# Kernel tuning notes

Measured on AMD Instinct MI355X. Metric: run time of the kernel, lower is better.

## Reference

```python
import jax, jax.numpy as jnp
from jax import lax
import numpy as np

B, T, F, H = 32, 512, 1024, 1024


def setup_inputs() -> dict:
    key = jax.random.key(0)
    ks = jax.random.split(key, 7)
    s = 0.02
    return {
        "x": jax.random.normal(ks[0], (B, T, F), dtype=jnp.float32),
        "W0": jax.random.normal(ks[1], (F, 4 * H), dtype=jnp.float32) * s,
        "U0": jax.random.normal(ks[2], (H, 4 * H), dtype=jnp.float32) * s,
        "b0": jax.random.normal(ks[3], (4 * H,), dtype=jnp.float32) * s,
        "W1": jax.random.normal(ks[4], (H, 4 * H), dtype=jnp.float32) * s,
        "U1": jax.random.normal(ks[5], (H, 4 * H), dtype=jnp.float32) * s,
        "b1": jax.random.normal(ks[6], (4 * H,), dtype=jnp.float32) * s,
    }


def _lstm(x, W, U, b):
    # x: [B, T, F] -> sequence outputs [B, T, H], final h, final c
    b_, t_, _ = x.shape
    h_dim = U.shape[0]
    # Precompute input projections for all timesteps (batched GEMM).
    xz = jnp.einsum('btf,fg->btg', x, W) + b  # [B, T, 4H]

    def step(carry, xz_t):
        h, c = carry
        z = xz_t + h @ U  # [B, 4H]
        i, f, g, o = jnp.split(z, 4, axis=-1)  # Keras gate order: i, f, c(g), o
        i = jax.nn.sigmoid(i)
        f = jax.nn.sigmoid(f)
        g = jnp.tanh(g)
        o = jax.nn.sigmoid(o)
        c = f * c + i * g
        h = o * jnp.tanh(c)
        return (h, c), h

    h0 = jnp.zeros((b_, h_dim), dtype=x.dtype)
    c0 = jnp.zeros((b_, h_dim), dtype=x.dtype)
    (h, c), hs = lax.scan(step, (h0, c0), jnp.swapaxes(xz, 0, 1))
    return jnp.swapaxes(hs, 0, 1), h, c


def reference(x, W0, U0, b0, W1, U1, b1):
    # Layer 0: return_sequences=True
    seq0, _, _ = _lstm(x, W0, U0, b0)
    # Layer 1: return_state=True -> (last_output, h, c); last_output == h
    _, h1, c1 = _lstm(seq0, W1, U1, b1)
    return (h1, h1, c1)
```

## Files before the change

### kernel.cpp

```cpp
#include <hip/hip_runtime.h>
#include <cstdint>


typedef __attribute__((ext_vector_type(8))) short bf16x8;
typedef __attribute__((ext_vector_type(4))) short s16x4;
typedef __attribute__((ext_vector_type(4))) float f32x4;
typedef __attribute__((ext_vector_type(2))) unsigned int u32x2;

#define XZ0_OFF   0ull
#define XF_OFF    134217728ull
#define W0F_OFF   167772160ull
#define U0F_OFF   176160768ull
#define W1F_OFF   184549376ull
#define WS_TOTAL  201326592ull
#define RING_OFF  XF_OFF
#define H1B_OFF   (XF_OFF + 524288ull)
#define FLG_OFF   (XF_OFF + 655360ull)

__device__ __forceinline__ float bf2f(short s) {
  unsigned int u = ((unsigned int)(unsigned short)s) << 16;
  return __builtin_bit_cast(float, u);
}
__device__ __forceinline__ short f2bf(float f) {
  unsigned int u = __builtin_bit_cast(unsigned int, f);
  u = (u + 0x7fffu + ((u >> 16) & 1u)) >> 16;
  return (short)u;
}
__device__ __forceinline__ void g2l16(const void* g, void* l) {
  __builtin_amdgcn_global_load_lds(
      (const __attribute__((address_space(1))) unsigned int*)g,
      (__attribute__((address_space(3))) unsigned int*)l, 16, 0, 0);
}
__device__ __forceinline__ float sigm(float x) { return 1.f / (1.f + __expf(-x)); }

__device__ __forceinline__ bf16x8 ld16_sc1(const short* p) {
  bf16x8 r;
  asm volatile("global_load_dwordx4 %0, %1, off sc1" : "=&v"(r) : "v"(p));
  return r;
}
__device__ __forceinline__ void st2_sc1(short* p, unsigned v) {
  asm volatile("global_store_short %0, %1, off sc1" :: "v"(p), "v"(v) : "memory");
}
__device__ __forceinline__ void st4_sc1(unsigned* p, unsigned v) {
  asm volatile("global_store_dword %0, %1, off sc1" :: "v"(p), "v"(v) : "memory");
}
#define VM_DRAIN asm volatile("s_waitcnt vmcnt(0)" ::: "memory")
#define SBAR __builtin_amdgcn_sched_barrier(0)

__global__ __launch_bounds__(256) void pack_x(const float* __restrict__ x,
                                              short* __restrict__ dst) {
  int gid = blockIdx.x * 256 + threadIdx.x;
  int lane = gid & 63;
  int unit = gid >> 6;
  int mtile = unit >> 5, kstep = unit & 31;
  int row = mtile * 16 + (lane & 15);
  int k0 = kstep * 32 + ((lane >> 4) << 3);
  const float* s = x + (size_t)row * 1024 + k0;
  bf16x8 v;
#pragma unroll
  for (int j = 0; j < 8; j++) v[j] = f2bf(s[j]);
  *(bf16x8*)(dst + (size_t)gid * 8) = v;
}

__global__ __launch_bounds__(256) void pack_w(const float* __restrict__ src0,
                                              const float* __restrict__ src1,
                                              int ksh, short* __restrict__ dst) {
  int gid = blockIdx.x * 256 + threadIdx.x;
  int lane = gid & 63;
  int unit = gid >> 6;
  int ntile = unit >> ksh;
  int kstep = unit & ((1 << ksh) - 1);
  int col = ntile * 16 + (lane & 15);
  int k0 = kstep * 32 + ((lane >> 4) << 3);
  const float* s = (k0 < 1024) ? src0 : src1;
  int kk = k0 & 1023;
  bf16x8 v;
#pragma unroll
  for (int j = 0; j < 8; j++) v[j] = f2bf(s[(size_t)(kk + j) * 4096 + col]);
  *(bf16x8*)(dst + (size_t)gid * 8) = v;
}

__global__ __launch_bounds__(256) void gemm_xw(const short* __restrict__ xf,
                                               const short* __restrict__ wf,
                                               short* __restrict__ outz) {
  extern __shared__ char smem[];

  int bid = blockIdx.x;
  int swz = (bid & 7) * 512 + (bid >> 3);
  int bn = swz >> 7;
  int bm = swz & 127;

  const int tid = threadIdx.x, wid = tid >> 6, lane = tid & 63;
  const int wm = wid >> 1, wn = wid & 1;
  f32x4 acc[4][4] = {};

  const short* xbase = xf + (size_t)(bm * 8) * 32 * 512;
  const short* wbase = wf + (size_t)(bn * 8) * 32 * 512;

  auto Abuf = [&](int buf) -> short* { return (short*)(smem + buf * 32768); };
  auto Bbuf = [&](int buf) -> short* { return (short*)(smem + 16384 + buf * 32768); };

  auto stage = [&](int buf, int kt) {
    short* A = Abuf(buf);
    short* B = Bbuf(buf);
#pragma unroll
    for (int i = 0; i < 4; i++) {
      int u = wid + 4 * i;
      int mt = u >> 1, ks = u & 1;
      int gk = kt * 2 + ks;
      g2l16(xbase + (size_t)(mt * 32 + gk) * 512 + lane * 8, A + u * 512);
      g2l16(wbase + (size_t)(mt * 32 + gk) * 512 + lane * 8, B + u * 512);
    }
  };

  stage(0, 0);
  __syncthreads();
  for (int kt = 0; kt < 16; kt++) {
    int buf = kt & 1;
    if (kt < 15) stage(buf ^ 1, kt + 1);
    const short* A = Abuf(buf) + (wm * 4) * 1024;
    const short* B = Bbuf(buf) + (wn * 4) * 1024;
#pragma unroll
    for (int ks = 0; ks < 2; ks++) {
      bf16x8 av[4], bv[4];
#pragma unroll
      for (int i = 0; i < 4; i++) av[i] = *(const bf16x8*)(A + (i * 2 + ks) * 512 + lane * 8);
#pragma unroll
      for (int j = 0; j < 4; j++) bv[j] = *(const bf16x8*)(B + (j * 2 + ks) * 512 + lane * 8);
#pragma unroll
      for (int i = 0; i < 4; i++)
#pragma unroll
        for (int j = 0; j < 4; j++)
          acc[i][j] = __builtin_amdgcn_mfma_f32_16x16x32_bf16(av[i], bv[j], acc[i][j], 0, 0, 0);
    }
    __syncthreads();
  }

  int rb = bm * 128 + wm * 64 + ((lane >> 4) << 2);
  int cb = bn * 128 + wn * 64 + (lane & 15);
#pragma unroll
  for (int i = 0; i < 4; i++)
#pragma unroll
    for (int j = 0; j < 4; j++)
#pragma unroll
      for (int r = 0; r < 4; r++) {
        size_t row = rb + i * 16 + r;
        int col = cb + j * 16;
        outz[row * 4096 + (size_t)(col & 1023) * 4 + (col >> 10)] = f2bf(acc[i][j][r]);
      }
}

__global__ __launch_bounds__(256, 1) void lstm_persist(
    const short* __restrict__ xz0, const short* __restrict__ u0f,
    const short* __restrict__ w1u1f, const float* __restrict__ b0,
    const float* __restrict__ b1, short* __restrict__ h0ring,
    short* __restrict__ h1buf, unsigned int* __restrict__ flags,
    float* __restrict__ out) {
  extern __shared__ char smem[];
  short* wlds = (short*)smem;
  float* red0 = (float*)(smem + 131072);
  float* red1 = (float*)(smem + 139264);

  const int wg = blockIdx.x;
  const int tid = threadIdx.x;
  const int wid = tid >> 6;
  const int lane = tid & 63;
  const bool l1 = (wg >= 128);
  const int u0 = (wg & 127) * 8;
  const int KS = l1 ? 64 : 32;
  const int ksh = l1 ? 6 : 5;
  const short* wf = l1 ? w1u1f : u0f;

  {
    int c = lane & 15;
    for (int u = wid; u < 2 * KS; u += 4) {
      int tau = u >> ksh;
      int s = u & (KS - 1);
      int gate = tau * 2 + (c >> 3);
      int gc = gate * 1024 + u0 + (c & 7);
      int lanep = (lane & 48) + (gc & 15);
      const short* src = wf + ((size_t)(((gc >> 4) << ksh) + s) * 64 + lanep) * 8;
      g2l16(src, wlds + (tau * KS + s) * 512);
    }
  }
  __syncthreads();

  const int bl = (tid & 127) >> 3;
  const int uu = tid & 7;
  const int lrow = bl >> 2, reg = bl & 3;
  float bias[4];
  {
    const float* bb = l1 ? b1 : b0;
#pragma unroll
    for (int g = 0; g < 4; g++) bias[g] = bb[g * 1024 + u0 + uu];
  }

  unsigned int* ownbase = flags + (l1 ? 256 : 0);
  unsigned int* othbase = flags + (l1 ? 0 : 256);

  auto pollq = [&](int q, unsigned own_t, unsigned oth_t) {
    if ((own_t | oth_t) == 0) return;
    const unsigned* po = ownbase + q * 128 + lane * 2;
    const unsigned* pe = othbase + q * 128 + lane * 2;
    for (int it = 0; it < (1 << 22); ++it) {
      u32x2 ov, ev;
      asm volatile(
          "global_load_dwordx2 %0, %2, off sc1\n\t"
          "global_load_dwordx2 %1, %3, off sc1\n\t"
          "s_waitcnt vmcnt(0)"
          : "=&v"(ov), "=&v"(ev)
          : "v"(po), "v"(pe)
          : "memory");
      if (__all(ov[0] >= own_t && ov[1] >= own_t &&
                ev[0] >= oth_t && ev[1] >= oth_t)) break;
      asm volatile("s_sleep 1");
    }
  };

  auto gates1 = [&](const float* rd, s16x4 xv, float& cst, short* hw,
                    bool dump, int g) {
    float z[4];
#pragma unroll
    for (int g4 = 0; g4 < 4; g4++) {
      int tau = g4 >> 1;
      int lp = lrow * 16 + (g4 & 1) * 8 + uu;
      float s = bias[g4] + bf2f(xv[g4]);
#pragma unroll
      for (int w4 = 0; w4 < 4; w4++)
        s += rd[((w4 * 2 + tau) * 64 + lp) * 4 + reg];
      z[g4] = s;
    }
    float gi = sigm(z[0]);
    float gf = sigm(z[1]);
    float gg = tanhf(z[2]);
    float go = sigm(z[3]);
    cst = gf * cst + gi * gg;
    float hv = go * tanhf(cst);
    st2_sc1(hw + (g * 16 + bl) * 1024 + u0 + uu,
            (unsigned)(unsigned short)f2bf(hv));
    if (dump) {
      int oi = (g * 16 + bl) * 1024 + u0 + uu;
      out[oi] = hv;
      out[32768 + oi] = hv;
      out[65536 + oi] = cst;
    }
  };

  if (!l1) {
    float c0 = 0.f, c1 = 0.f;
    auto mini = [&](int g, int t, float& cst) {
      const short* ap = h0ring + (size_t)((t - 1) & 7) * 32768 +
                        (g * 16 + (lane & 15)) * 1024 + (wid << 8) +
                        ((lane >> 4) << 3);
      bf16x8 a[8];
#pragma unroll
      for (int ks = 0; ks < 8; ks++) a[ks] = ld16_sc1(ap + ks * 32);
      s16x4 xv = {0, 0, 0, 0};
      if (tid < 128)
        xv = *(const s16x4*)(xz0 +
              ((size_t)((g * 16 + bl) * 512 + t) * 1024 + u0 + uu) * 4);
      SBAR; VM_DRAIN; SBAR;
      f32x4 acc[2] = {};
#pragma unroll
      for (int ks = 0; ks < 8; ks++) {
        bf16x8 bt0 = *(const bf16x8*)(wlds + (wid * 8 + ks) * 512 + lane * 8);
        bf16x8 bt1 = *(const bf16x8*)(wlds + (32 + wid * 8 + ks) * 512 + lane * 8);
        acc[0] = __builtin_amdgcn_mfma_f32_16x16x32_bf16(a[ks], bt0, acc[0], 0, 0, 0);
        acc[1] = __builtin_amdgcn_mfma_f32_16x16x32_bf16(a[ks], bt1, acc[1], 0, 0, 0);
      }
      float* rd = g ? red1 : red0;
#pragma unroll
      for (int tau = 0; tau < 2; tau++)
        *(f32x4*)(rd + ((wid * 2 + tau) * 64 + lane) * 4) = acc[tau];
      __syncthreads();
      if (tid < 128) {
        gates1(rd, xv, cst, h0ring + (size_t)(t & 7) * 32768, false, g);
      } else if (wid == 2 && g == 0) {
        pollq(1, (unsigned)t, (t >= 8) ? (unsigned)(t - 7) : 0u);
      } else if (wid == 3 && g == 1 && t < 511) {
        pollq(0, (unsigned)(t + 1), (t + 1 >= 8) ? (unsigned)(t - 6) : 0u);
      }
      VM_DRAIN;
      __syncthreads();
      if (tid == 0) st4_sc1(ownbase + g * 128 + (wg & 127), (unsigned)(t + 1));
    };
    for (int t = 0; t < 512; ++t) { mini(0, t, c0); mini(1, t, c1); }
  } else {
    float c0 = 0.f, c1 = 0.f;
    if (wid == 3) pollq(0, 0u, 1u);
    __syncthreads();
    auto mini = [&](int g, int t, float& cst) {
      const short* Ab = (wid < 2) ? (h0ring + (size_t)(t & 7) * 32768)
                                  : (h1buf + (size_t)((t - 1) & 1) * 32768);
      const short* ap = Ab + (g * 16 + (lane & 15)) * 1024 + ((wid & 1) << 9) +
                        ((lane >> 4) << 3);
      bf16x8 a[2][8];
#pragma unroll
      for (int half = 0; half < 2; half++)
#pragma unroll
        for (int ks = 0; ks < 8; ks++)
          a[half][ks] = ld16_sc1(ap + half * 256 + ks * 32);
      SBAR; VM_DRAIN; SBAR;
      f32x4 acc[2] = {};
#pragma unroll
      for (int half = 0; half < 2; half++) {
        const int rb = wid * 16 + half * 8;
#pragma unroll
        for (int ks = 0; ks < 8; ks++) {
          bf16x8 bt0 = *(const bf16x8*)(wlds + (rb + ks) * 512 + lane * 8);
          bf16x8 bt1 = *(const bf16x8*)(wlds + (64 + rb + ks) * 512 + lane * 8);
          acc[0] = __builtin_amdgcn_mfma_f32_16x16x32_bf16(a[half][ks], bt0, acc[0], 0, 0, 0);
          acc[1] = __builtin_amdgcn_mfma_f32_16x16x32_bf16(a[half][ks], bt1, acc[1], 0, 0, 0);
        }
      }
      float* rd = g ? red1 : red0;
#pragma unroll
      for (int tau = 0; tau < 2; tau++)
        *(f32x4*)(rd + ((wid * 2 + tau) * 64 + lane) * 4) = acc[tau];
      __syncthreads();
      if (tid < 128) {
        s16x4 zv = {0, 0, 0, 0};
        gates1(rd, zv, cst, h1buf + (size_t)(t & 1) * 32768, t == 511, g);
      } else if (wid == 2 && g == 0) {
        pollq(1, (unsigned)t, (unsigned)(t + 1));
      } else if (wid == 3 && g == 1 && t < 511) {
        pollq(0, (unsigned)(t + 1), (unsigned)(t + 2));
      }
      VM_DRAIN;
      __syncthreads();
      if (tid == 0) st4_sc1(ownbase + g * 128 + (wg & 127), (unsigned)(t + 1));
    };
    for (int t = 0; t < 512; ++t) { mini(0, t, c0); mini(1, t, c1); }
  }
}

extern "C" void kernel_launch(void* const* d_in, const int* in_sizes, int n_in,
                              void* d_out, int out_size, void* d_ws, size_t ws_size,
                              hipStream_t stream) {
  const float* x  = (const float*)d_in[0];
  const float* W0 = (const float*)d_in[1];
  const float* U0 = (const float*)d_in[2];
  const float* b0 = (const float*)d_in[3];
  const float* W1 = (const float*)d_in[4];
  const float* U1 = (const float*)d_in[5];
  const float* b1 = (const float*)d_in[6];
  char* ws = (char*)d_ws;
  if (ws_size < WS_TOTAL) return;

  short* xz0p = (short*)(ws + XZ0_OFF);
  short* xfp  = (short*)(ws + XF_OFF);
  short* w0fp = (short*)(ws + W0F_OFF);
  short* u0fp = (short*)(ws + U0F_OFF);
  short* w1fp = (short*)(ws + W1F_OFF);
  short* ringp = (short*)(ws + RING_OFF);
  short* h1p   = (short*)(ws + H1B_OFF);
  unsigned int* flagp = (unsigned int*)(ws + FLG_OFF);
  float* outp = (float*)d_out;

  (void)hipFuncSetAttribute((const void*)gemm_xw,
      hipFuncAttributeMaxDynamicSharedMemorySize, 65536);
  (void)hipFuncSetAttribute((const void*)lstm_persist,
      hipFuncAttributeMaxDynamicSharedMemorySize, 147456);

  hipLaunchKernelGGL(pack_x, dim3(8192), dim3(256), 0, stream, x, xfp);
  hipLaunchKernelGGL(pack_w, dim3(2048), dim3(256), 0, stream, W0, W0, 5, w0fp);
  hipLaunchKernelGGL(pack_w, dim3(2048), dim3(256), 0, stream, U0, U0, 5, u0fp);
  hipLaunchKernelGGL(pack_w, dim3(4096), dim3(256), 0, stream, W1, U1, 6, w1fp);
  hipLaunchKernelGGL(gemm_xw, dim3(4096), dim3(256), 65536, stream, xfp, w0fp, xz0p);

  (void)hipMemsetAsync(ws + RING_OFF, 0, 524288 + 131072 + 4096, stream);

  const short* xz0c = xz0p;
  const short* u0fc = u0fp;
  const short* w1fc = w1fp;
  void* kargs[9] = {(void*)&xz0c, (void*)&u0fc, (void*)&w1fc,
                    (void*)&b0,   (void*)&b1,
                    (void*)&ringp, (void*)&h1p, (void*)&flagp, (void*)&outp};
  (void)hipLaunchCooperativeKernel((const void*)lstm_persist, dim3(256), dim3(256),
                                   kargs, 147456u, stream);
}
```

Before: 3.919 ms.

## Prefetch next mini-step hidden-state loads before flag publish in LSTM recurrence

Restructures the per-timestep loop of both LSTM layers so that the A-operand (hidden state) loads for the next mini-step are issued right after the gate computation. Only the older stores are then drained with partial vmcnt waits, and raw s_barrier with lgkmcnt waits replaces full __syncthreads. Polling of neighbour progress flags moves to the start of each mini-step on wave 2, so the dependency wait sits right before use. The goal is to overlap global-load latency with the flag publish and barrier. The risk is subtle: the next loads are issued before the peers' flags have been checked, which can read stale ring data, and the hand-counted vmcnt values must match the number of outstanding ops exactly.

New measurement: 7.704 ms. +96.6%, slower.

```diff
diff --git a/kernel.cpp b/kernel.cpp
--- a/kernel.cpp
+++ b/kernel.cpp
@@ -38,6 +38,11 @@
   asm volatile("global_load_dwordx4 %0, %1, off sc1" : "=&v"(r) : "v"(p));
   return r;
 }
+__device__ __forceinline__ s16x4 ld8_plain(const short* p) {
+  s16x4 r;
+  asm volatile("global_load_dwordx2 %0, %1, off" : "=&v"(r) : "v"(p));
+  return r;
+}
 __device__ __forceinline__ void st2_sc1(short* p, unsigned v) {
   asm volatile("global_store_short %0, %1, off sc1" :: "v"(p), "v"(v) : "memory");
 }
@@ -45,7 +50,12 @@
   asm volatile("global_store_dword %0, %1, off sc1" :: "v"(p), "v"(v) : "memory");
 }
 #define VM_DRAIN asm volatile("s_waitcnt vmcnt(0)" ::: "memory")
+#define VM_W1    asm volatile("s_waitcnt vmcnt(1)" ::: "memory")
+#define VM_W9    asm volatile("s_waitcnt vmcnt(9)" ::: "memory")
+#define VM_W16   asm volatile("s_waitcnt vmcnt(16)" ::: "memory")
+#define LGKM0    asm volatile("s_waitcnt lgkmcnt(0)" ::: "memory")
 #define SBAR __builtin_amdgcn_sched_barrier(0)
+#define RBAR __builtin_amdgcn_s_barrier()
 
 __global__ __launch_bounds__(256) void pack_x(const float* __restrict__ x,
                                               short* __restrict__ dst) {
@@ -236,72 +246,91 @@
     float go = sigm(z[3]);
     cst = gf * cst + gi * gg;
     float hv = go * tanhf(cst);
-    st2_sc1(hw + (g * 16 + bl) * 1024 + u0 + uu,
-            (unsigned)(unsigned short)f2bf(hv));
     if (dump) {
       int oi = (g * 16 + bl) * 1024 + u0 + uu;
       out[oi] = hv;
       out[32768 + oi] = hv;
       out[65536 + oi] = cst;
     }
+    st2_sc1(hw + (g * 16 + bl) * 1024 + u0 + uu,
+            (unsigned)(unsigned short)f2bf(hv));
   };
 
   if (!l1) {
-    float c0 = 0.f, c1 = 0.f;
-    auto mini = [&](int g, int t, float& cst) {
+    bf16x8 A[8];
+    s16x4 xv = {0, 0, 0, 0};
+    auto issueA = [&](int g, int t) {
       const short* ap = h0ring + (size_t)((t - 1) & 7) * 32768 +
                         (g * 16 + (lane & 15)) * 1024 + (wid << 8) +
                         ((lane >> 4) << 3);
-      bf16x8 a[8];
-#pragma unroll
-      for (int ks = 0; ks < 8; ks++) a[ks] = ld16_sc1(ap + ks * 32);
-      s16x4 xv = {0, 0, 0, 0};
+#pragma unroll
+      for (int ks = 0; ks < 8; ks++) A[ks] = ld16_sc1(ap + ks * 32);
       if (tid < 128)
-        xv = *(const s16x4*)(xz0 +
-              ((size_t)((g * 16 + bl) * 512 + t) * 1024 + u0 + uu) * 4);
-      SBAR; VM_DRAIN; SBAR;
-      f32x4 acc[2] = {};
+        xv = ld8_plain(xz0 +
+             ((size_t)((g * 16 + bl) * 512 + t) * 1024 + u0 + uu) * 4);
+    };
+    auto body = [&](int g, int t, float& cst, int pq, unsigned po, unsigned pt,
+                    bool donext, int ng, int nt, bool first) {
+      if (wid == 2) pollq(pq, po, pt);
+      if (first) { VM_DRAIN; }
+      else if (wid == 0) { VM_W1; }
+      else { VM_DRAIN; }
+      SBAR;
+      f32x4 acc0 = {}, acc1 = {};
 #pragma unroll
       for (int ks = 0; ks < 8; ks++) {
         bf16x8 bt0 = *(const bf16x8*)(wlds + (wid * 8 + ks) * 512 + lane * 8);
         bf16x8 bt1 = *(const bf16x8*)(wlds + (32 + wid * 8 + ks) * 512 + lane * 8);
-        acc[0] = __builtin_amdgcn_mfma_f32_16x16x32_bf16(a[ks], bt0, acc[0], 0, 0, 0);
-        acc[1] = __builtin_amdgcn_mfma_f32_16x16x32_bf16(a[ks], bt1, acc[1], 0, 0, 0);
+        acc0 = __builtin_amdgcn_mfma_f32_16x16x32_bf16(A[ks], bt0, acc0, 0, 0, 0);
+        acc1 = __builtin_amdgcn_mfma_f32_16x16x32_bf16(A[ks], bt1, acc1, 0, 0, 0);
       }
       float* rd = g ? red1 : red0;
-#pragma unroll
-      for (int tau = 0; tau < 2; tau++)
-        *(f32x4*)(rd + ((wid * 2 + tau) * 64 + lane) * 4) = acc[tau];
-      __syncthreads();
+      *(f32x4*)(rd + ((wid * 2 + 0) * 64 + lane) * 4) = acc0;
+      *(f32x4*)(rd + ((wid * 2 + 1) * 64 + lane) * 4) = acc1;
+      LGKM0; RBAR; SBAR;
+      s16x4 xcur = xv;
       if (tid < 128) {
-        gates1(rd, xv, cst, h0ring + (size_t)(t & 7) * 32768, false, g);
-      } else if (wid == 2 && g == 0) {
-        pollq(1, (unsigned)t, (t >= 8) ? (unsigned)(t - 7) : 0u);
-      } else if (wid == 3 && g == 1 && t < 511) {
-        pollq(0, (unsigned)(t + 1), (t + 1 >= 8) ? (unsigned)(t - 6) : 0u);
+        gates1(rd, xcur, cst, h0ring + (size_t)(t & 7) * 32768, false, g);
+        if (donext) issueA(ng, nt);
+      } else {
+        if (donext) issueA(ng, nt);
       }
-      VM_DRAIN;
-      __syncthreads();
-      if (tid == 0) st4_sc1(ownbase + g * 128 + (wg & 127), (unsigned)(t + 1));
+      if (donext) { VM_W9; } else { VM_DRAIN; }
+      SBAR; RBAR;
+      if (tid == 0)
+        st4_sc1(ownbase + g * 128 + (wg & 127), (unsigned)(t + 1));
     };
-    for (int t = 0; t < 512; ++t) { mini(0, t, c0); mini(1, t, c1); }
+    issueA(0, 0);
+    float c0 = 0.f, c1 = 0.f;
+    for (int t = 0; t < 512; ++t) {
+      body(0, t, c0, 1, (unsigned)t, (t >= 8) ? (unsigned)(t - 7) : 0u,
+           true, 1, t, t == 0);
+      bool dn = (t < 511);
+      body(1, t, c1, 0, dn ? (unsigned)(t + 1) : 0u,
+           dn ? ((t + 1 >= 8) ? (unsigned)(t - 6) : 0u) : 0u,
+           dn, 0, t + 1, false);
+    }
   } else {
-    float c0 = 0.f, c1 = 0.f;
-    if (wid == 3) pollq(0, 0u, 1u);
-    __syncthreads();
-    auto mini = [&](int g, int t, float& cst) {
+    bf16x8 A1[2][8];
+    auto issueA1 = [&](int g, int t) {
       const short* Ab = (wid < 2) ? (h0ring + (size_t)(t & 7) * 32768)
                                   : (h1buf + (size_t)((t - 1) & 1) * 32768);
       const short* ap = Ab + (g * 16 + (lane & 15)) * 1024 + ((wid & 1) << 9) +
                         ((lane >> 4) << 3);
-      bf16x8 a[2][8];
 #pragma unroll
       for (int half = 0; half < 2; half++)
 #pragma unroll
         for (int ks = 0; ks < 8; ks++)
-          a[half][ks] = ld16_sc1(ap + half * 256 + ks * 32);
-      SBAR; VM_DRAIN; SBAR;
-      f32x4 acc[2] = {};
+          A1[half][ks] = ld16_sc1(ap + half * 256 + ks * 32);
+    };
+    auto body = [&](int g, int t, float& cst, int pq, unsigned po, unsigned pt,
+                    bool donext, int ng, int nt, bool first) {
+      if (wid == 2) pollq(pq, po, pt);
+      if (first) { VM_DRAIN; }
+      else if (wid == 0) { VM_W1; }
+      else { VM_DRAIN; }
+      SBAR;
+      f32x4 acc0 = {}, acc1 = {};
 #pragma unroll
       for (int half = 0; half < 2; half++) {
         const int rb = wid * 16 + half * 8;
@@ -309,28 +338,36 @@
         for (int ks = 0; ks < 8; ks++) {
           bf16x8 bt0 = *(const bf16x8*)(wlds + (rb + ks) * 512 + lane * 8);
           bf16x8 bt1 = *(const bf16x8*)(wlds + (64 + rb + ks) * 512 + lane * 8);
-          acc[0] = __builtin_amdgcn_mfma_f32_16x16x32_bf16(a[half][ks], bt0, acc[0], 0, 0, 0);
-          acc[1] = __builtin_amdgcn_mfma_f32_16x16x32_bf16(a[half][ks], bt1, acc[1], 0, 0, 0);
+          acc0 = __builtin_amdgcn_mfma_f32_16x16x32_bf16(A1[half][ks], bt0, acc0, 0, 0, 0);
+          acc1 = __builtin_amdgcn_mfma_f32_16x16x32_bf16(A1[half][ks], bt1, acc1, 0, 0, 0);
         }
       }
       float* rd = g ? red1 : red0;
-#pragma unroll
-      for (int tau = 0; tau < 2; tau++)
-        *(f32x4*)(rd + ((wid * 2 + tau) * 64 + lane) * 4) = acc[tau];
-      __syncthreads();
+      *(f32x4*)(rd + ((wid * 2 + 0) * 64 + lane) * 4) = acc0;
+      *(f32x4*)(rd + ((wid * 2 + 1) * 64 + lane) * 4) = acc1;
+      LGKM0; RBAR; SBAR;
       if (tid < 128) {
         s16x4 zv = {0, 0, 0, 0};
         gates1(rd, zv, cst, h1buf + (size_t)(t & 1) * 32768, t == 511, g);
-      } else if (wid == 2 && g == 0) {
-        pollq(1, (unsigned)t, (unsigned)(t + 1));
-      } else if (wid == 3 && g == 1 && t < 511) {
-        pollq(0, (unsigned)(t + 1), (unsigned)(t + 2));
+        if (donext) issueA1(ng, nt);
+      } else {
+        if (donext) issueA1(ng, nt);
       }
-      VM_DRAIN;
-      __syncthreads();
-      if (tid == 0) st4_sc1(ownbase + g * 128 + (wg & 127), (unsigned)(t + 1));
+      if (donext) { VM_W16; } else { VM_DRAIN; }
+      SBAR; RBAR;
+      if (tid == 0)
+        st4_sc1(ownbase + g * 128 + (wg & 127), (unsigned)(t + 1));
     };
-    for (int t = 0; t < 512; ++t) { mini(0, t, c0); mini(1, t, c1); }
+    if (wid == 2) pollq(0, 0u, 1u);
+    __syncthreads();
+    issueA1(0, 0);
+    float c0 = 0.f, c1 = 0.f;
+    for (int t = 0; t < 512; ++t) {
+      body(0, t, c0, 1, (unsigned)t, (unsigned)(t + 1), true, 1, t, t == 0);
+      bool dn = (t < 511);
+      body(1, t, c1, 0, dn ? (unsigned)(t + 1) : 0u,
+           dn ? (unsigned)(t + 2) : 0u, dn, 0, t + 1, false);
+    }
   }
 }
 
```

## Merge two batch half-steps into one full-batch step per timestep

Applied to the files above, without the earlier changes.

The persistent LSTM kernel used to process each timestep as two 16-row batch halves, each with its own flag publish and poll round. It now handles all 32 batch rows in a single pass per timestep, with four MFMA accumulators per wave and one flag set per layer. Layer 1 also waits on only the first half of its loads before starting MFMAs. This halves the number of cross-workgroup synchronisation rounds per step at the cost of more registers and less overlap between the two halves. Polling now happens after the flag store instead of overlapping with the gate computation.

Result: slower. 5.687 ms (+45.1%).

```diff
diff --git a/kernel.cpp b/kernel.cpp
--- a/kernel.cpp
+++ b/kernel.cpp
@@ -38,6 +38,11 @@
   asm volatile("global_load_dwordx4 %0, %1, off sc1" : "=&v"(r) : "v"(p));
   return r;
 }
+__device__ __forceinline__ s16x4 ld8_plain(const short* p) {
+  s16x4 r;
+  asm volatile("global_load_dwordx2 %0, %1, off" : "=&v"(r) : "v"(p));
+  return r;
+}
 __device__ __forceinline__ void st2_sc1(short* p, unsigned v) {
   asm volatile("global_store_short %0, %1, off sc1" :: "v"(p), "v"(v) : "memory");
 }
@@ -45,7 +50,16 @@
   asm volatile("global_store_dword %0, %1, off sc1" :: "v"(p), "v"(v) : "memory");
 }
 #define VM_DRAIN asm volatile("s_waitcnt vmcnt(0)" ::: "memory")
+#define VM_W16   asm volatile("s_waitcnt vmcnt(16)" ::: "memory")
 #define SBAR __builtin_amdgcn_sched_barrier(0)
+
+struct Frag8 { bf16x8 f0, f1, f2, f3, f4, f5, f6, f7; };
+#define LD8(F, B) do { \
+  (F).f0 = ld16_sc1((B));       (F).f1 = ld16_sc1((B) + 32);  \
+  (F).f2 = ld16_sc1((B) + 64);  (F).f3 = ld16_sc1((B) + 96);  \
+  (F).f4 = ld16_sc1((B) + 128); (F).f5 = ld16_sc1((B) + 160); \
+  (F).f6 = ld16_sc1((B) + 192); (F).f7 = ld16_sc1((B) + 224); \
+} while (0)
 
 __global__ __launch_bounds__(256) void pack_x(const float* __restrict__ x,
                                               short* __restrict__ dst) {
@@ -158,8 +172,7 @@
     float* __restrict__ out) {
   extern __shared__ char smem[];
   short* wlds = (short*)smem;
-  float* red0 = (float*)(smem + 131072);
-  float* red1 = (float*)(smem + 139264);
+  float* red = (float*)(smem + 131072);
 
   const int wg = blockIdx.x;
   const int tid = threadIdx.x;
@@ -185,23 +198,24 @@
   }
   __syncthreads();
 
-  const int bl = (tid & 127) >> 3;
-  const int uu = tid & 7;
-  const int lrow = bl >> 2, reg = bl & 3;
+  const int un = tid & 7;
+  const int r1 = (tid & 127) >> 3;
+  const int r2 = r1 + 16;
   float bias[4];
   {
     const float* bb = l1 ? b1 : b0;
 #pragma unroll
-    for (int g = 0; g < 4; g++) bias[g] = bb[g * 1024 + u0 + uu];
+    for (int g4 = 0; g4 < 4; g4++) bias[g4] = bb[g4 * 1024 + u0 + un];
   }
-
-  unsigned int* ownbase = flags + (l1 ? 256 : 0);
-  unsigned int* othbase = flags + (l1 ? 0 : 256);
-
-  auto pollq = [&](int q, unsigned own_t, unsigned oth_t) {
+  float cA = 0.f, cB = 0.f;
+
+  unsigned int* ownf = flags + (l1 ? 128 : 0);
+  unsigned int* othf = flags + (l1 ? 0 : 128);
+
+  auto pollq = [&](unsigned own_t, unsigned oth_t) {
     if ((own_t | oth_t) == 0) return;
-    const unsigned* po = ownbase + q * 128 + lane * 2;
-    const unsigned* pe = othbase + q * 128 + lane * 2;
+    const unsigned* po = ownf + lane * 2;
+    const unsigned* pe = othf + lane * 2;
     for (int it = 0; it < (1 << 22); ++it) {
       u32x2 ov, ev;
       asm volatile(
@@ -217,17 +231,18 @@
     }
   };
 
-  auto gates1 = [&](const float* rd, s16x4 xv, float& cst, short* hw,
-                    bool dump, int g) {
+  auto gaterow = [&](int r, s16x4 xv, float& cst, short* hw, bool dump) {
+    const int mt = r >> 4, bl = r & 15;
+    const int reg = bl & 3;
     float z[4];
 #pragma unroll
     for (int g4 = 0; g4 < 4; g4++) {
       int tau = g4 >> 1;
-      int lp = lrow * 16 + (g4 & 1) * 8 + uu;
+      int lp = (bl >> 2) * 16 + (g4 & 1) * 8 + un;
       float s = bias[g4] + bf2f(xv[g4]);
 #pragma unroll
       for (int w4 = 0; w4 < 4; w4++)
-        s += rd[((w4 * 2 + tau) * 64 + lp) * 4 + reg];
+        s += red[((w4 * 4 + mt * 2 + tau) * 64 + lp) * 4 + reg];
       z[g4] = s;
     }
     float gi = sigm(z[0]);
@@ -236,101 +251,123 @@
     float go = sigm(z[3]);
     cst = gf * cst + gi * gg;
     float hv = go * tanhf(cst);
-    st2_sc1(hw + (g * 16 + bl) * 1024 + u0 + uu,
-            (unsigned)(unsigned short)f2bf(hv));
     if (dump) {
-      int oi = (g * 16 + bl) * 1024 + u0 + uu;
+      int oi = r * 1024 + u0 + un;
       out[oi] = hv;
       out[32768 + oi] = hv;
       out[65536 + oi] = cst;
     }
+    st2_sc1(hw + r * 1024 + u0 + un, (unsigned)(unsigned short)f2bf(hv));
   };
 
   if (!l1) {
-    float c0 = 0.f, c1 = 0.f;
-    auto mini = [&](int g, int t, float& cst) {
+    for (int t = 0; t < 512; ++t) {
       const short* ap = h0ring + (size_t)((t - 1) & 7) * 32768 +
-                        (g * 16 + (lane & 15)) * 1024 + (wid << 8) +
-                        ((lane >> 4) << 3);
-      bf16x8 a[8];
-#pragma unroll
-      for (int ks = 0; ks < 8; ks++) a[ks] = ld16_sc1(ap + ks * 32);
-      s16x4 xv = {0, 0, 0, 0};
-      if (tid < 128)
-        xv = *(const s16x4*)(xz0 +
-              ((size_t)((g * 16 + bl) * 512 + t) * 1024 + u0 + uu) * 4);
+                        (lane & 15) * 1024 + (wid << 8) + ((lane >> 4) << 3);
+      Frag8 Fa, Fb;
+      LD8(Fa, ap);
+      LD8(Fb, ap + 16384);
+      s16x4 xvA = {0, 0, 0, 0}, xvB = {0, 0, 0, 0};
+      if (tid < 128) {
+        xvA = ld8_plain(xz0 + ((size_t)(r1 * 512 + t) * 1024 + u0 + un) * 4);
+        xvB = ld8_plain(xz0 + ((size_t)(r2 * 512 + t) * 1024 + u0 + un) * 4);
+      }
       SBAR; VM_DRAIN; SBAR;
-      f32x4 acc[2] = {};
+      f32x4 a00 = {}, a01 = {}, a10 = {}, a11 = {};
 #pragma unroll
       for (int ks = 0; ks < 8; ks++) {
         bf16x8 bt0 = *(const bf16x8*)(wlds + (wid * 8 + ks) * 512 + lane * 8);
         bf16x8 bt1 = *(const bf16x8*)(wlds + (32 + wid * 8 + ks) * 512 + lane * 8);
-        acc[0] = __builtin_amdgcn_mfma_f32_16x16x32_bf16(a[ks], bt0, acc[0], 0, 0, 0);
-        acc[1] = __builtin_amdgcn_mfma_f32_16x16x32_bf16(a[ks], bt1, acc[1], 0, 0, 0);
-      }
-      float* rd = g ? red1 : red0;
-#pragma unroll
-      for (int tau = 0; tau < 2; tau++)
-        *(f32x4*)(rd + ((wid * 2 + tau) * 64 + lane) * 4) = acc[tau];
+        bf16x8 fa = ks == 0 ? Fa.f0 : ks == 1 ? Fa.f1 : ks == 2 ? Fa.f2 :
+                    ks == 3 ? Fa.f3 : ks == 4 ? Fa.f4 : ks == 5 ? Fa.f5 :
+                    ks == 6 ? Fa.f6 : Fa.f7;
+        bf16x8 fb = ks == 0 ? Fb.f0 : ks == 1 ? Fb.f1 : ks == 2 ? Fb.f2 :
+                    ks == 3 ? Fb.f3 : ks == 4 ? Fb.f4 : ks == 5 ? Fb.f5 :
+                    ks == 6 ? Fb.f6 : Fb.f7;
+        a00 = __builtin_amdgcn_mfma_f32_16x16x32_bf16(fa, bt0, a00, 0, 0, 0);
+        a01 = __builtin_amdgcn_mfma_f32_16x16x32_bf16(fa, bt1, a01, 0, 0, 0);
+        a10 = __builtin_amdgcn_mfma_f32_16x16x32_bf16(fb, bt0, a10, 0, 0, 0);
+        a11 = __builtin_amdgcn_mfma_f32_16x16x32_bf16(fb, bt1, a11, 0, 0, 0);
+      }
+      *(f32x4*)(red + ((wid * 4 + 0) * 64 + lane) * 4) = a00;
+      *(f32x4*)(red + ((wid * 4 + 1) * 64 + lane) * 4) = a01;
+      *(f32x4*)(red + ((wid * 4 + 2) * 64 + lane) * 4) = a10;
+      *(f32x4*)(red + ((wid * 4 + 3) * 64 + lane) * 4) = a11;
       __syncthreads();
       if (tid < 128) {
-        gates1(rd, xv, cst, h0ring + (size_t)(t & 7) * 32768, false, g);
-      } else if (wid == 2 && g == 0) {
-        pollq(1, (unsigned)t, (t >= 8) ? (unsigned)(t - 7) : 0u);
-      } else if (wid == 3 && g == 1 && t < 511) {
-        pollq(0, (unsigned)(t + 1), (t + 1 >= 8) ? (unsigned)(t - 6) : 0u);
-      }
-      VM_DRAIN;
-      __syncthreads();
-      if (tid == 0) st4_sc1(ownbase + g * 128 + (wg & 127), (unsigned)(t + 1));
-    };
-    for (int t = 0; t < 512; ++t) { mini(0, t, c0); mini(1, t, c1); }
+        short* hw = h0ring + (size_t)(t & 7) * 32768;
+        gaterow(r1, xvA, cA, hw, false);
+        gaterow(r2, xvB, cB, hw, false);
+      }
+      __syncthreads();
+      if (tid == 0) st4_sc1(ownf + (wg & 127), (unsigned)(t + 1));
+      if (wid == 2 && t < 511)
+        pollq((unsigned)(t + 1), (t + 1 >= 8) ? (unsigned)(t - 6) : 0u);
+      __syncthreads();
+    }
   } else {
-    float c0 = 0.f, c1 = 0.f;
-    if (wid == 3) pollq(0, 0u, 1u);
+    if (wid == 2) pollq(0u, 1u);
     __syncthreads();
-    auto mini = [&](int g, int t, float& cst) {
+    for (int t = 0; t < 512; ++t) {
       const short* Ab = (wid < 2) ? (h0ring + (size_t)(t & 7) * 32768)
                                   : (h1buf + (size_t)((t - 1) & 1) * 32768);
-      const short* ap = Ab + (g * 16 + (lane & 15)) * 1024 + ((wid & 1) << 9) +
+      const short* ap = Ab + (lane & 15) * 1024 + ((wid & 1) << 9) +
                         ((lane >> 4) << 3);
-      bf16x8 a[2][8];
-#pragma unroll
-      for (int half = 0; half < 2; half++)
-#pragma unroll
-        for (int ks = 0; ks < 8; ks++)
-          a[half][ks] = ld16_sc1(ap + half * 256 + ks * 32);
+      Frag8 Fa, Fb, Fc, Fd;
+      LD8(Fa, ap);
+      LD8(Fb, ap + 16384);
+      LD8(Fc, ap + 256);
+      LD8(Fd, ap + 256 + 16384);
+      SBAR; VM_W16; SBAR;
+      f32x4 a00 = {}, a01 = {}, a10 = {}, a11 = {};
+#pragma unroll
+      for (int ks = 0; ks < 8; ks++) {
+        bf16x8 bt0 = *(const bf16x8*)(wlds + (wid * 16 + ks) * 512 + lane * 8);
+        bf16x8 bt1 = *(const bf16x8*)(wlds + (64 + wid * 16 + ks) * 512 + lane * 8);
+        bf16x8 fa = ks == 0 ? Fa.f0 : ks == 1 ? Fa.f1 : ks == 2 ? Fa.f2 :
+                    ks == 3 ? Fa.f3 : ks == 4 ? Fa.f4 : ks == 5 ? Fa.f5 :
+                    ks == 6 ? Fa.f6 : Fa.f7;
+        bf16x8 fb = ks == 0 ? Fb.f0 : ks == 1 ? Fb.f1 : ks == 2 ? Fb.f2 :
+                    ks == 3 ? Fb.f3 : ks == 4 ? Fb.f4 : ks == 5 ? Fb.f5 :
+                    ks == 6 ? Fb.f6 : Fb.f7;
+        a00 = __builtin_amdgcn_mfma_f32_16x16x32_bf16(fa, bt0, a00, 0, 0, 0);
+        a01 = __builtin_amdgcn_mfma_f32_16x16x32_bf16(fa, bt1, a01, 0, 0, 0);
+        a10 = __builtin_amdgcn_mfma_f32_16x16x32_bf16(fb, bt0, a10, 0, 0, 0);
+        a11 = __builtin_amdgcn_mfma_f32_16x16x32_bf16(fb, bt1, a11, 0, 0, 0);
+      }
       SBAR; VM_DRAIN; SBAR;
-      f32x4 acc[2] = {};
-#pragma unroll
-      for (int half = 0; half < 2; half++) {
-        const int rb = wid * 16 + half * 8;
-#pragma unroll
-        for (int ks = 0; ks < 8; ks++) {
-          bf16x8 bt0 = *(const bf16x8*)(wlds + (rb + ks) * 512 + lane * 8);
-          bf16x8 bt1 = *(const bf16x8*)(wlds + (64 + rb + ks) * 512 + lane * 8);
-          acc[0] = __builtin_amdgcn_mfma_f32_16x16x32_bf16(a[half][ks], bt0, acc[0], 0, 0, 0);
-          acc[1] = __builtin_amdgcn_mfma_f32_16x16x32_bf16(a[half][ks], bt1, acc[1], 0, 0, 0);
-        }
-      }
-      float* rd = g ? red1 : red0;
-#pragma unroll
-      for (int tau = 0; tau < 2; tau++)
-        *(f32x4*)(rd + ((wid * 2 + tau) * 64 + lane) * 4) = acc[tau];
+#pragma unroll
+      for (int ks = 0; ks < 8; ks++) {
+        bf16x8 bt0 = *(const bf16x8*)(wlds + (wid * 16 + 8 + ks) * 512 + lane * 8);
+        bf16x8 bt1 = *(const bf16x8*)(wlds + (64 + wid * 16 + 8 + ks) * 512 + lane * 8);
+        bf16x8 fc = ks == 0 ? Fc.f0 : ks == 1 ? Fc.f1 : ks == 2 ? Fc.f2 :
+                    ks == 3 ? Fc.f3 : ks == 4 ? Fc.f4 : ks == 5 ? Fc.f5 :
+                    ks == 6 ? Fc.f6 : Fc.f7;
+        bf16x8 fd = ks == 0 ? Fd.f0 : ks == 1 ? Fd.f1 : ks == 2 ? Fd.f2 :
+                    ks == 3 ? Fd.f3 : ks == 4 ? Fd.f4 : ks == 5 ? Fd.f5 :
+                    ks == 6 ? Fd.f6 : Fd.f7;
+        a00 = __builtin_amdgcn_mfma_f32_16x16x32_bf16(fc, bt0, a00, 0, 0, 0);
+        a01 = __builtin_amdgcn_mfma_f32_16x16x32_bf16(fc, bt1, a01, 0, 0, 0);
+        a10 = __builtin_amdgcn_mfma_f32_16x16x32_bf16(fd, bt0, a10, 0, 0, 0);
+        a11 = __builtin_amdgcn_mfma_f32_16x16x32_bf16(fd, bt1, a11, 0, 0, 0);
+      }
+      *(f32x4*)(red + ((wid * 4 + 0) * 64 + lane) * 4) = a00;
+      *(f32x4*)(red + ((wid * 4 + 1) * 64 + lane) * 4) = a01;
+      *(f32x4*)(red + ((wid * 4 + 2) * 64 + lane) * 4) = a10;
+      *(f32x4*)(red + ((wid * 4 + 3) * 64 + lane) * 4) = a11;
       __syncthreads();
       if (tid < 128) {
+        short* hw = h1buf + (size_t)(t & 1) * 32768;
         s16x4 zv = {0, 0, 0, 0};
-        gates1(rd, zv, cst, h1buf + (size_t)(t & 1) * 32768, t == 511, g);
-      } else if (wid == 2 && g == 0) {
-        pollq(1, (unsigned)t, (unsigned)(t + 1));
-      } else if (wid == 3 && g == 1 && t < 511) {
-        pollq(0, (unsigned)(t + 1), (unsigned)(t + 2));
-      }
-      VM_DRAIN;
-      __syncthreads();
-      if (tid == 0) st4_sc1(ownbase + g * 128 + (wg & 127), (unsigned)(t + 1));
-    };
-    for (int t = 0; t < 512; ++t) { mini(0, t, c0); mini(1, t, c1); }
+        gaterow(r1, zv, cA, hw, t == 511);
+        gaterow(r2, zv, cB, hw, t == 511);
+      }
+      __syncthreads();
+      if (tid == 0) st4_sc1(ownf + (wg & 127), (unsigned)(t + 1));
+      if (wid == 2 && t < 511)
+        pollq((unsigned)(t + 1), (unsigned)(t + 2));
+      __syncthreads();
+    }
   }
 }
 
```

## Replace block-level flag barriers with per-wave flags and 8-deep layer-1 ring

Applied to the files above, without the earlier changes.

Each wavefront now publishes its own completion flag and polls only the producer flags it needs before loading its slice of h. This removes the second __syncthreads per mini-step and the dedicated polling waves. Layer 1's h buffer grows from double-buffered to an 8-deep ring, so layer 0 can run further ahead. Gate computation is spread across all four waves (32 lanes each) instead of two. In exchange there are four times as many flag stores and more polling traffic, and the finer-grained memory ordering carries correctness risk.

After: 4.868 ms. +24.2%, slower.

```diff
diff --git a/kernel.cpp b/kernel.cpp
--- a/kernel.cpp
+++ b/kernel.cpp
@@ -6,6 +6,7 @@
 typedef __attribute__((ext_vector_type(4))) short s16x4;
 typedef __attribute__((ext_vector_type(4))) float f32x4;
 typedef __attribute__((ext_vector_type(2))) unsigned int u32x2;
+typedef __attribute__((ext_vector_type(4))) unsigned int u32x4;
 
 #define XZ0_OFF   0ull
 #define XF_OFF    134217728ull
@@ -13,9 +14,9 @@
 #define U0F_OFF   176160768ull
 #define W1F_OFF   184549376ull
 #define WS_TOTAL  201326592ull
-#define RING_OFF  XF_OFF
-#define H1B_OFF   (XF_OFF + 524288ull)
-#define FLG_OFF   (XF_OFF + 655360ull)
+#define H0R_OFF   XF_OFF
+#define H1R_OFF   (XF_OFF + 524288ull)
+#define FLG_OFF   (XF_OFF + 1048576ull)
 
 __device__ __forceinline__ float bf2f(short s) {
   unsigned int u = ((unsigned int)(unsigned short)s) << 16;
@@ -38,6 +39,11 @@
   asm volatile("global_load_dwordx4 %0, %1, off sc1" : "=&v"(r) : "v"(p));
   return r;
 }
+__device__ __forceinline__ s16x4 ld8_plain(const short* p) {
+  s16x4 r;
+  asm volatile("global_load_dwordx2 %0, %1, off" : "=&v"(r) : "v"(p));
+  return r;
+}
 __device__ __forceinline__ void st2_sc1(short* p, unsigned v) {
   asm volatile("global_store_short %0, %1, off sc1" :: "v"(p), "v"(v) : "memory");
 }
@@ -46,6 +52,17 @@
 }
 #define VM_DRAIN asm volatile("s_waitcnt vmcnt(0)" ::: "memory")
 #define SBAR __builtin_amdgcn_sched_barrier(0)
+
+struct Frag8 { bf16x8 f0, f1, f2, f3, f4, f5, f6, f7; };
+#define LD8(F, B) do { \
+  (F).f0 = ld16_sc1((B));       (F).f1 = ld16_sc1((B) + 32);  \
+  (F).f2 = ld16_sc1((B) + 64);  (F).f3 = ld16_sc1((B) + 96);  \
+  (F).f4 = ld16_sc1((B) + 128); (F).f5 = ld16_sc1((B) + 160); \
+  (F).f6 = ld16_sc1((B) + 192); (F).f7 = ld16_sc1((B) + 224); \
+} while (0)
+#define FSEL(F, ks) (ks == 0 ? (F).f0 : ks == 1 ? (F).f1 : ks == 2 ? (F).f2 : \
+                     ks == 3 ? (F).f3 : ks == 4 ? (F).f4 : ks == 5 ? (F).f5 : \
+                     ks == 6 ? (F).f6 : (F).f7)
 
 __global__ __launch_bounds__(256) void pack_x(const float* __restrict__ x,
                                               short* __restrict__ dst) {
@@ -154,7 +171,7 @@
     const short* __restrict__ xz0, const short* __restrict__ u0f,
     const short* __restrict__ w1u1f, const float* __restrict__ b0,
     const float* __restrict__ b1, short* __restrict__ h0ring,
-    short* __restrict__ h1buf, unsigned int* __restrict__ flags,
+    short* __restrict__ h1ring, unsigned int* __restrict__ flags,
     float* __restrict__ out) {
   extern __shared__ char smem[];
   short* wlds = (short*)smem;
@@ -163,7 +180,7 @@
 
   const int wg = blockIdx.x;
   const int tid = threadIdx.x;
-  const int wid = tid >> 6;
+  const int w = tid >> 6;
   const int lane = tid & 63;
   const bool l1 = (wg >= 128);
   const int u0 = (wg & 127) * 8;
@@ -173,7 +190,7 @@
 
   {
     int c = lane & 15;
-    for (int u = wid; u < 2 * KS; u += 4) {
+    for (int u = w; u < 2 * KS; u += 4) {
       int tau = u >> ksh;
       int s = u & (KS - 1);
       int gate = tau * 2 + (c >> 3);
@@ -185,49 +202,65 @@
   }
   __syncthreads();
 
-  const int bl = (tid & 127) >> 3;
-  const int uu = tid & 7;
-  const int lrow = bl >> 2, reg = bl & 3;
+  const int un = lane & 7;
   float bias[4];
   {
     const float* bb = l1 ? b1 : b0;
 #pragma unroll
-    for (int g = 0; g < 4; g++) bias[g] = bb[g * 1024 + u0 + uu];
+    for (int g4 = 0; g4 < 4; g4++) bias[g4] = bb[g4 * 1024 + u0 + un];
   }
 
-  unsigned int* ownbase = flags + (l1 ? 256 : 0);
-  unsigned int* othbase = flags + (l1 ? 0 : 256);
-
-  auto pollq = [&](int q, unsigned own_t, unsigned oth_t) {
-    if ((own_t | oth_t) == 0) return;
-    const unsigned* po = ownbase + q * 128 + lane * 2;
-    const unsigned* pe = othbase + q * 128 + lane * 2;
+  auto poll0 = [&](int g, int t) {
+    if (t == 0) return;
+    const unsigned tgt = (unsigned)t;
+    const unsigned lagt = (t >= 8) ? (unsigned)(t - 7) : 0u;
+    const unsigned* pp = flags + (unsigned)(g * 128 + w * 32) * 4 + lane * 2;
+    const unsigned* pl = flags + (unsigned)((2 + g) * 128 + w * 32 + (lane >> 1)) * 4 + (lane & 1);
     for (int it = 0; it < (1 << 22); ++it) {
-      u32x2 ov, ev;
+      u32x2 ov; unsigned lv;
       asm volatile(
           "global_load_dwordx2 %0, %2, off sc1\n\t"
-          "global_load_dwordx2 %1, %3, off sc1\n\t"
+          "global_load_dword %1, %3, off sc1\n\t"
           "s_waitcnt vmcnt(0)"
-          : "=&v"(ov), "=&v"(ev)
-          : "v"(po), "v"(pe)
-          : "memory");
-      if (__all(ov[0] >= own_t && ov[1] >= own_t &&
-                ev[0] >= oth_t && ev[1] >= oth_t)) break;
+          : "=&v"(ov), "=&v"(lv) : "v"(pp), "v"(pl) : "memory");
+      if (__all(ov[0] >= tgt && ov[1] >= tgt && lv >= lagt)) break;
       asm volatile("s_sleep 1");
     }
   };
-
-  auto gates1 = [&](const float* rd, s16x4 xv, float& cst, short* hw,
-                    bool dump, int g) {
+  auto poll1 = [&](int g, int t) {
+    unsigned tgt;
+    const unsigned* pp;
+    if (w < 2) {
+      tgt = (unsigned)(t + 1);
+      pp = flags + (unsigned)(g * 128 + w * 64) * 4 + lane * 4;
+    } else {
+      if (t == 0) return;
+      tgt = (unsigned)t;
+      pp = flags + (unsigned)((2 + g) * 128 + (w - 2) * 64) * 4 + lane * 4;
+    }
+    for (int it = 0; it < (1 << 22); ++it) {
+      u32x4 v;
+      asm volatile(
+          "global_load_dwordx4 %0, %1, off sc1\n\t"
+          "s_waitcnt vmcnt(0)"
+          : "=&v"(v) : "v"(pp) : "memory");
+      if (__all(v[0] >= tgt && v[1] >= tgt && v[2] >= tgt && v[3] >= tgt)) break;
+      asm volatile("s_sleep 1");
+    }
+  };
+
+  auto gates = [&](const float* rd, s16x4 xv, float& cst, short* hw,
+                   bool dump, int g) {
+    const int bl = w * 4 + (lane >> 3);
     float z[4];
 #pragma unroll
     for (int g4 = 0; g4 < 4; g4++) {
       int tau = g4 >> 1;
-      int lp = lrow * 16 + (g4 & 1) * 8 + uu;
+      int lp = (bl >> 2) * 16 + (g4 & 1) * 8 + un;
       float s = bias[g4] + bf2f(xv[g4]);
 #pragma unroll
       for (int w4 = 0; w4 < 4; w4++)
-        s += rd[((w4 * 2 + tau) * 64 + lp) * 4 + reg];
+        s += rd[((w4 * 2 + tau) * 64 + lp) * 4 + (bl & 3)];
       z[g4] = s;
     }
     float gi = sigm(z[0]);
@@ -236,99 +269,96 @@
     float go = sigm(z[3]);
     cst = gf * cst + gi * gg;
     float hv = go * tanhf(cst);
-    st2_sc1(hw + (g * 16 + bl) * 1024 + u0 + uu,
-            (unsigned)(unsigned short)f2bf(hv));
     if (dump) {
-      int oi = (g * 16 + bl) * 1024 + u0 + uu;
+      int oi = (g * 16 + bl) * 1024 + u0 + un;
       out[oi] = hv;
       out[32768 + oi] = hv;
       out[65536 + oi] = cst;
     }
+    st2_sc1(hw + (g * 16 + bl) * 1024 + u0 + un,
+            (unsigned)(unsigned short)f2bf(hv));
+  };
+
+  auto release = [&](int g, int t) {
+    if (lane == 0)
+      st4_sc1(flags + (unsigned)(((l1 ? 2 : 0) + g) * 128 + (wg & 127)) * 4 + w,
+              (unsigned)(t + 1));
   };
 
   if (!l1) {
     float c0 = 0.f, c1 = 0.f;
     auto mini = [&](int g, int t, float& cst) {
+      poll0(g, t);
       const short* ap = h0ring + (size_t)((t - 1) & 7) * 32768 +
-                        (g * 16 + (lane & 15)) * 1024 + (wid << 8) +
+                        (g * 16 + (lane & 15)) * 1024 + (w << 8) +
                         ((lane >> 4) << 3);
-      bf16x8 a[8];
-#pragma unroll
-      for (int ks = 0; ks < 8; ks++) a[ks] = ld16_sc1(ap + ks * 32);
+      Frag8 Fa;
+      LD8(Fa, ap);
       s16x4 xv = {0, 0, 0, 0};
-      if (tid < 128)
-        xv = *(const s16x4*)(xz0 +
-              ((size_t)((g * 16 + bl) * 512 + t) * 1024 + u0 + uu) * 4);
+      if (lane < 32) {
+        int bl = w * 4 + (lane >> 3);
+        xv = ld8_plain(xz0 +
+             (((size_t)((g * 16 + bl) * 512 + t)) * 1024 + u0 + un) * 4);
+      }
       SBAR; VM_DRAIN; SBAR;
-      f32x4 acc[2] = {};
+      f32x4 a0 = {}, a1 = {};
 #pragma unroll
       for (int ks = 0; ks < 8; ks++) {
-        bf16x8 bt0 = *(const bf16x8*)(wlds + (wid * 8 + ks) * 512 + lane * 8);
-        bf16x8 bt1 = *(const bf16x8*)(wlds + (32 + wid * 8 + ks) * 512 + lane * 8);
-        acc[0] = __builtin_amdgcn_mfma_f32_16x16x32_bf16(a[ks], bt0, acc[0], 0, 0, 0);
-        acc[1] = __builtin_amdgcn_mfma_f32_16x16x32_bf16(a[ks], bt1, acc[1], 0, 0, 0);
+        bf16x8 bt0 = *(const bf16x8*)(wlds + (w * 8 + ks) * 512 + lane * 8);
+        bf16x8 bt1 = *(const bf16x8*)(wlds + (32 + w * 8 + ks) * 512 + lane * 8);
+        bf16x8 fa = FSEL(Fa, ks);
+        a0 = __builtin_amdgcn_mfma_f32_16x16x32_bf16(fa, bt0, a0, 0, 0, 0);
+        a1 = __builtin_amdgcn_mfma_f32_16x16x32_bf16(fa, bt1, a1, 0, 0, 0);
       }
       float* rd = g ? red1 : red0;
-#pragma unroll
-      for (int tau = 0; tau < 2; tau++)
-        *(f32x4*)(rd + ((wid * 2 + tau) * 64 + lane) * 4) = acc[tau];
+      *(f32x4*)(rd + ((w * 2 + 0) * 64 + lane) * 4) = a0;
+      *(f32x4*)(rd + ((w * 2 + 1) * 64 + lane) * 4) = a1;
       __syncthreads();
-      if (tid < 128) {
-        gates1(rd, xv, cst, h0ring + (size_t)(t & 7) * 32768, false, g);
-      } else if (wid == 2 && g == 0) {
-        pollq(1, (unsigned)t, (t >= 8) ? (unsigned)(t - 7) : 0u);
-      } else if (wid == 3 && g == 1 && t < 511) {
-        pollq(0, (unsigned)(t + 1), (t + 1 >= 8) ? (unsigned)(t - 6) : 0u);
-      }
+      if (lane < 32)
+        gates(rd, xv, cst, h0ring + (size_t)(t & 7) * 32768, false, g);
       VM_DRAIN;
-      __syncthreads();
-      if (tid == 0) st4_sc1(ownbase + g * 128 + (wg & 127), (unsigned)(t + 1));
+      release(g, t);
     };
     for (int t = 0; t < 512; ++t) { mini(0, t, c0); mini(1, t, c1); }
   } else {
     float c0 = 0.f, c1 = 0.f;
-    if (wid == 3) pollq(0, 0u, 1u);
-    __syncthreads();
     auto mini = [&](int g, int t, float& cst) {
-      const short* Ab = (wid < 2) ? (h0ring + (size_t)(t & 7) * 32768)
-                                  : (h1buf + (size_t)((t - 1) & 1) * 32768);
-      const short* ap = Ab + (g * 16 + (lane & 15)) * 1024 + ((wid & 1) << 9) +
+      poll1(g, t);
+      const short* Ab = (w < 2) ? (h0ring + (size_t)(t & 7) * 32768)
+                                : (h1ring + (size_t)((t - 1) & 7) * 32768);
+      const short* ap = Ab + (g * 16 + (lane & 15)) * 1024 + ((w & 1) << 9) +
                         ((lane >> 4) << 3);
-      bf16x8 a[2][8];
-#pragma unroll
-      for (int half = 0; half < 2; half++)
-#pragma unroll
-        for (int ks = 0; ks < 8; ks++)
-          a[half][ks] = ld16_sc1(ap + half * 256 + ks * 32);
+      Frag8 Fa, Fc;
+      LD8(Fa, ap);
+      LD8(Fc, ap + 256);
       SBAR; VM_DRAIN; SBAR;
-      f32x4 acc[2] = {};
-#pragma unroll
-      for (int half = 0; half < 2; half++) {
-        const int rb = wid * 16 + half * 8;
-#pragma unroll
-        for (int ks = 0; ks < 8; ks++) {
-          bf16x8 bt0 = *(const bf16x8*)(wlds + (rb + ks) * 512 + lane * 8);
-          bf16x8 bt1 = *(const bf16x8*)(wlds + (64 + rb + ks) * 512 + lane * 8);
-          acc[0] = __builtin_amdgcn_mfma_f32_16x16x32_bf16(a[half][ks], bt0, acc[0], 0, 0, 0);
-          acc[1] = __builtin_amdgcn_mfma_f32_16x16x32_bf16(a[half][ks], bt1, acc[1], 0, 0, 0);
-        }
+      f32x4 a0 = {}, a1 = {};
+#pragma unroll
+      for (int ks = 0; ks < 8; ks++) {
+        bf16x8 bt0 = *(const bf16x8*)(wlds + (w * 16 + ks) * 512 + lane * 8);
+        bf16x8 bt1 = *(const bf16x8*)(wlds + (64 + w * 16 + ks) * 512 + lane * 8);
+        bf16x8 fa = FSEL(Fa, ks);
+        a0 = __builtin_amdgcn_mfma_f32_16x16x32_bf16(fa, bt0, a0, 0, 0, 0);
+        a1 = __builtin_amdgcn_mfma_f32_16x16x32_bf16(fa, bt1, a1, 0, 0, 0);
+      }
+#pragma unroll
+      for (int ks = 0; ks < 8; ks++) {
+        bf16x8 bt0 = *(const bf16x8*)(wlds + (w * 16 + 8 + ks) * 512 + lane * 8);
+        bf16x8 bt1 = *(const bf16x8*)(wlds + (64 + w * 16 + 8 + ks) * 512 + lane * 8);
+        bf16x8 fc = FSEL(Fc, ks);
+        a0 = __builtin_amdgcn_mfma_f32_16x16x32_bf16(fc, bt0, a0, 0, 0, 0);
+        a1 = __builtin_amdgcn_mfma_f32_16x16x32_bf16(fc, bt1, a1, 0, 0, 0);
       }
       float* rd = g ? red1 : red0;
-#pragma unroll
-      for (int tau = 0; tau < 2; tau++)
-        *(f32x4*)(rd + ((wid * 2 + tau) * 64 + lane) * 4) = acc[tau];
+      *(f32x4*)(rd + ((w * 2 + 0) * 64 + lane) * 4) = a0;
+      *(f32x4*)(rd + ((w * 2 + 1) * 64 + lane) * 4) = a1;
       __syncthreads();
-      if (tid < 128) {
+      if (lane < 32) {
         s16x4 zv = {0, 0, 0, 0};
-        gates1(rd, zv, cst, h1buf + (size_t)(t & 1) * 32768, t == 511, g);
-      } else if (wid == 2 && g == 0) {
-        pollq(1, (unsigned)t, (unsigned)(t + 1));
-      } else if (wid == 3 && g == 1 && t < 511) {
-        pollq(0, (unsigned)(t + 1), (unsigned)(t + 2));
+        gates(rd, zv, cst, h1ring + (size_t)(t & 7) * 32768, t == 511, g);
       }
       VM_DRAIN;
-      __syncthreads();
-      if (tid == 0) st4_sc1(ownbase + g * 128 + (wg & 127), (unsigned)(t + 1));
+      release(g, t);
     };
     for (int t = 0; t < 512; ++t) { mini(0, t, c0); mini(1, t, c1); }
   }
@@ -352,8 +382,8 @@
   short* w0fp = (short*)(ws + W0F_OFF);
   short* u0fp = (short*)(ws + U0F_OFF);
   short* w1fp = (short*)(ws + W1F_OFF);
-  short* ringp = (short*)(ws + RING_OFF);
-  short* h1p   = (short*)(ws + H1B_OFF);
+  short* h0rp = (short*)(ws + H0R_OFF);
+  short* h1rp = (short*)(ws + H1R_OFF);
   unsigned int* flagp = (unsigned int*)(ws + FLG_OFF);
   float* outp = (float*)d_out;
 
@@ -368,14 +398,14 @@
   hipLaunchKernelGGL(pack_w, dim3(4096), dim3(256), 0, stream, W1, U1, 6, w1fp);
   hipLaunchKernelGGL(gemm_xw, dim3(4096), dim3(256), 65536, stream, xfp, w0fp, xz0p);
 
-  (void)hipMemsetAsync(ws + RING_OFF, 0, 524288 + 131072 + 4096, stream);
+  (void)hipMemsetAsync(ws + H0R_OFF, 0, 524288 + 524288 + 8192, stream);
 
   const short* xz0c = xz0p;
   const short* u0fc = u0fp;
   const short* w1fc = w1fp;
   void* kargs[9] = {(void*)&xz0c, (void*)&u0fc, (void*)&w1fc,
                     (void*)&b0,   (void*)&b1,
-                    (void*)&ringp, (void*)&h1p, (void*)&flagp, (void*)&outp};
+                    (void*)&h0rp, (void*)&h1rp, (void*)&flagp, (void*)&outp};
   (void)hipLaunchCooperativeKernel((const void*)lstm_persist, dim3(256), dim3(256),
                                    kargs, 147456u, stream);
 }
```
